# Kernel optimization log

Measured on AMD Instinct MI355X. Metric: run time of the kernel, lower is better.

## Reference

```python
import jax, jax.numpy as jnp
import numpy as np

B, IN, OUT, P = 512, 4096, 4096, 4
BITS = 4
MAX_INT = float(2 ** (BITS - 1) - 1)  # 7.0


def setup_inputs() -> dict:
    key = jax.random.key(0)
    k1, k2, k3, k4 = jax.random.split(key, 4)
    x = jax.random.normal(k1, (B, IN), dtype=jnp.float32)
    # Cached LFSR-generated pseudo-random matrix, values normalized to [-1, 1]
    U = jax.random.uniform(k2, (OUT * IN, P), dtype=jnp.float32, minval=-1.0, maxval=1.0)
    # 4-bit quantized projection: integers in [-7, 7] stored as float
    q = jnp.round(jnp.clip(jax.random.normal(k3, (P,), dtype=jnp.float32) * 3.0, -MAX_INT, MAX_INT))
    b = jax.random.normal(k4, (OUT,), dtype=jnp.float32)
    return {"x": x, "U": U, "q": q, "b": b, "exponent": 0}


def reference(x, U, q, b, exponent):
    # dequantize: t_hat = q / max_int * 2^exponent  (shared-exponent 4-bit dequant)
    scale = jnp.float32(2.0) ** exponent
    t_hat = q / MAX_INT * scale                      # [P]
    # reconstruct full weight: W = U @ t_hat, reshape to (out, in)
    w = (U @ t_hat).reshape(OUT, IN)                 # [OUT, IN]
    # original layer forward (nn.Linear): y = x @ W^T + b
    return x @ w.T + b                               # [B, OUT]
```

## Files before the change

kernel.cpp:

```cpp
#include <hip/hip_runtime.h>
#include <hip/hip_bf16.h>

typedef unsigned short ushort_t;
typedef unsigned int uint_t;
typedef __attribute__((ext_vector_type(4))) float f32x4;
typedef __attribute__((ext_vector_type(8))) short bf16x8;

#define B_DIM 512
#define IN_DIM 4096
#define OUT_DIM 4096
#define BN 64
#define BK 32
#define KSPLIT 8

__device__ __forceinline__ ushort_t f2bf(float f) {
    union { float f; uint_t u; } v; v.f = f;
    uint_t r = v.u + 0x7fffu + ((v.u >> 16) & 1u);
    return (ushort_t)(r >> 16);
}

__device__ __forceinline__ void async_copy16(void* lds, const void* g) {
    __builtin_amdgcn_global_load_lds(
        (const __attribute__((address_space(1))) uint_t*)g,
        (__attribute__((address_space(3))) uint_t*)lds, 16, 0, 0);
}

__global__ __launch_bounds__(256) void conv_x(const float4* __restrict__ X4,
                                              ushort_t* __restrict__ Xb) {
    size_t i = (size_t)blockIdx.x * 256 + threadIdx.x;
    float4 a = X4[i];
    ushort_t r[4] = { f2bf(a.x), f2bf(a.y), f2bf(a.z), f2bf(a.w) };
    *(uint2*)(Xb + i * 4) = *(const uint2*)r;
}

__global__ __launch_bounds__(256, 2) void gemm_fused(
    const ushort_t* __restrict__ Xb,
    const float4* __restrict__ U4,
    const float* __restrict__ q,
    const int* __restrict__ expo,
    float* __restrict__ part)
{
    const int K = IN_DIM, N = OUT_DIM, M = B_DIM;
    __shared__ ushort_t sX[512 * 32];
    __shared__ ushort_t sU[64 * 32];

    const int tid  = threadIdx.x;
    const int lane = tid & 63;
    const int wave = tid >> 6;
    const int n0 = blockIdx.x * BN;
    const int kz = blockIdx.y;
    const int kseg = K / KSPLIT;
    const size_t kbase = (size_t)kz * kseg;

    const float scale = exp2f((float)expo[0]) * (1.0f / 7.0f);
    const float t0 = q[0] * scale, t1 = q[1] * scale,
                t2 = q[2] * scale, t3 = q[3] * scale;

    const int xrow = tid >> 2;
    const int xcol = (tid & 3) * 8;
    const ushort_t* gx = Xb + (size_t)xrow * K + kbase + xcol;
    ushort_t* lx = sX + tid * 8;

    const int nb = tid >> 4;
    const int kp = tid & 15;
    const float4* gu = U4 + (size_t)(n0 + nb) * K + kbase + 2 * kp;
    uint_t* lu = (uint_t*)sU + nb * 16 + kp;

    const int quad = lane >> 4;
    const int r16  = lane & 15;
    const ushort_t* fa = sX + (wave * 128 + r16) * 32 + quad * 8;
    const ushort_t* fb = sU + r16 * 32 + quad * 8;

    f32x4 acc[8][4] = {};

    const int nsteps = kseg / BK;
    for (int s = 0; s < nsteps; ++s) {
#pragma unroll
        for (int p = 0; p < 8; ++p)
            async_copy16(lx + p * 2048, gx + (size_t)p * 64 * K);
        gx += BK;
#pragma unroll
        for (int r = 0; r < 4; ++r) {
            const float4* g = gu + (size_t)r * 16 * K;
            float4 ua = g[0], ub = g[1];
            float w0 = ua.x * t0 + ua.y * t1 + ua.z * t2 + ua.w * t3;
            float w1 = ub.x * t0 + ub.y * t1 + ub.z * t2 + ub.w * t3;
            lu[r * 256] = (uint_t)f2bf(w0) | ((uint_t)f2bf(w1) << 16);
        }
        gu += BK;
        __syncthreads();

        bf16x8 bv[4];
#pragma unroll
        for (int j = 0; j < 4; ++j)
            bv[j] = *(const bf16x8*)(fb + j * 16 * 32);
#pragma unroll
        for (int i = 0; i < 8; ++i) {
            bf16x8 av = *(const bf16x8*)(fa + i * 16 * 32);
#pragma unroll
            for (int j = 0; j < 4; ++j)
                acc[i][j] = __builtin_amdgcn_mfma_f32_16x16x32_bf16(
                    av, bv[j], acc[i][j], 0, 0, 0);
        }
        __syncthreads();
    }

    float* outp = part + (size_t)kz * M * N;
#pragma unroll
    for (int i = 0; i < 8; ++i) {
        const int mrow = wave * 128 + i * 16 + quad * 4;
#pragma unroll
        for (int j = 0; j < 4; ++j) {
            const int ncol = n0 + j * 16 + r16;
            float* o = outp + (size_t)mrow * N + ncol;
#pragma unroll
            for (int r = 0; r < 4; ++r)
                o[(size_t)r * N] = acc[i][j][r];
        }
    }
}

__global__ __launch_bounds__(256) void reduce_bias(const float4* __restrict__ part,
                                                   const float4* __restrict__ bias,
                                                   float4* __restrict__ out) {
    const int MN4 = (B_DIM * OUT_DIM) / 4;
    int i = blockIdx.x * 256 + threadIdx.x;
    float4 bb = bias[i & 1023];
    float sx = bb.x, sy = bb.y, sz = bb.z, sw = bb.w;
#pragma unroll
    for (int k = 0; k < KSPLIT; ++k) {
        float4 p = part[i + (size_t)k * MN4];
        sx += p.x; sy += p.y; sz += p.z; sw += p.w;
    }
    float4 o; o.x = sx; o.y = sy; o.z = sz; o.w = sw;
    out[i] = o;
}

extern "C" void kernel_launch(void* const* d_in, const int* in_sizes, int n_in,
                              void* d_out, int out_size, void* d_ws, size_t ws_size,
                              hipStream_t stream) {
    const float* x    = (const float*)d_in[0];
    const float* U    = (const float*)d_in[1];
    const float* q    = (const float*)d_in[2];
    const float* b    = (const float*)d_in[3];
    const int*   expo = (const int*)d_in[4];
    float* out = (float*)d_out;

    char* ws = (char*)d_ws;
    float*    prt = (float*)ws;
    ushort_t* Xb  = (ushort_t*)(ws + 67108864);

    conv_x<<<2048, 256, 0, stream>>>((const float4*)x, Xb);
    gemm_fused<<<dim3(64, KSPLIT), 256, 0, stream>>>(Xb, (const float4*)U,
                                                     q, expo, prt);
    reduce_bias<<<2048, 256, 0, stream>>>((const float4*)prt, (const float4*)b,
                                          (float4*)out);
}
```

Baseline: 418.8 us.

## Widen GEMM tile to 128 columns with 512 threads and store bf16 partials

The fused GEMM block grows from 64 to 128 output columns and from 256 to 512 threads arranged as a 4x2 wave grid, so each X tile loaded into LDS feeds twice as many columns. This halves the number of blocks and the total X traffic. The split-K partial sums are now written as bf16 instead of fp32, halving partial write and reduce-read traffic. In exchange, partials are rounded to bf16 before the reduction, which adds accuracy loss, and the grid drops to 256 blocks, which may reduce occupancy on a 256-CU device.

```diff
diff --git a/kernel.cpp b/kernel.cpp
--- a/kernel.cpp
+++ b/kernel.cpp
@@ -9,7 +9,7 @@
 #define B_DIM 512
 #define IN_DIM 4096
 #define OUT_DIM 4096
-#define BN 64
+#define BN 128
 #define BK 32
 #define KSPLIT 8
 
@@ -33,20 +33,22 @@
     *(uint2*)(Xb + i * 4) = *(const uint2*)r;
 }
 
-__global__ __launch_bounds__(256, 2) void gemm_fused(
+__global__ __launch_bounds__(512, 2) void gemm_fused(
     const ushort_t* __restrict__ Xb,
     const float4* __restrict__ U4,
     const float* __restrict__ q,
     const int* __restrict__ expo,
-    float* __restrict__ part)
+    ushort_t* __restrict__ part)
 {
     const int K = IN_DIM, N = OUT_DIM, M = B_DIM;
     __shared__ ushort_t sX[512 * 32];
-    __shared__ ushort_t sU[64 * 32];
+    __shared__ ushort_t sU[128 * 32];
 
     const int tid  = threadIdx.x;
     const int lane = tid & 63;
     const int wave = tid >> 6;
+    const int wrow = (wave & 3) * 128;
+    const int wcol = (wave >> 2) * 64;
     const int n0 = blockIdx.x * BN;
     const int kz = blockIdx.y;
     const int kseg = K / KSPLIT;
@@ -68,24 +70,24 @@
 
     const int quad = lane >> 4;
     const int r16  = lane & 15;
-    const ushort_t* fa = sX + (wave * 128 + r16) * 32 + quad * 8;
-    const ushort_t* fb = sU + r16 * 32 + quad * 8;
+    const ushort_t* fa = sX + (wrow + r16) * 32 + quad * 8;
+    const ushort_t* fb = sU + (wcol + r16) * 32 + quad * 8;
 
     f32x4 acc[8][4] = {};
 
     const int nsteps = kseg / BK;
     for (int s = 0; s < nsteps; ++s) {
 #pragma unroll
-        for (int p = 0; p < 8; ++p)
-            async_copy16(lx + p * 2048, gx + (size_t)p * 64 * K);
+        for (int p = 0; p < 4; ++p)
+            async_copy16(lx + p * 4096, gx + (size_t)p * 128 * K);
         gx += BK;
 #pragma unroll
         for (int r = 0; r < 4; ++r) {
-            const float4* g = gu + (size_t)r * 16 * K;
+            const float4* g = gu + (size_t)r * 32 * K;
             float4 ua = g[0], ub = g[1];
             float w0 = ua.x * t0 + ua.y * t1 + ua.z * t2 + ua.w * t3;
             float w1 = ub.x * t0 + ub.y * t1 + ub.z * t2 + ub.w * t3;
-            lu[r * 256] = (uint_t)f2bf(w0) | ((uint_t)f2bf(w1) << 16);
+            lu[r * 512] = (uint_t)f2bf(w0) | ((uint_t)f2bf(w1) << 16);
         }
         gu += BK;
         __syncthreads();
@@ -105,22 +107,22 @@
         __syncthreads();
     }
 
-    float* outp = part + (size_t)kz * M * N;
+    ushort_t* outp = part + (size_t)kz * M * N;
 #pragma unroll
     for (int i = 0; i < 8; ++i) {
-        const int mrow = wave * 128 + i * 16 + quad * 4;
+        const int mrow = wrow + i * 16 + quad * 4;
 #pragma unroll
         for (int j = 0; j < 4; ++j) {
-            const int ncol = n0 + j * 16 + r16;
-            float* o = outp + (size_t)mrow * N + ncol;
+            const int ncol = n0 + wcol + j * 16 + r16;
+            ushort_t* o = outp + (size_t)mrow * N + ncol;
 #pragma unroll
             for (int r = 0; r < 4; ++r)
-                o[(size_t)r * N] = acc[i][j][r];
+                o[(size_t)r * N] = f2bf(acc[i][j][r]);
         }
     }
 }
 
-__global__ __launch_bounds__(256) void reduce_bias(const float4* __restrict__ part,
+__global__ __launch_bounds__(256) void reduce_bias(const uint2* __restrict__ partb,
                                                    const float4* __restrict__ bias,
                                                    float4* __restrict__ out) {
     const int MN4 = (B_DIM * OUT_DIM) / 4;
@@ -129,8 +131,11 @@
     float sx = bb.x, sy = bb.y, sz = bb.z, sw = bb.w;
 #pragma unroll
     for (int k = 0; k < KSPLIT; ++k) {
-        float4 p = part[i + (size_t)k * MN4];
-        sx += p.x; sy += p.y; sz += p.z; sw += p.w;
+        uint2 p = partb[i + (size_t)k * MN4];
+        sx += __uint_as_float(p.x << 16);
+        sy += __uint_as_float(p.x & 0xffff0000u);
+        sz += __uint_as_float(p.y << 16);
+        sw += __uint_as_float(p.y & 0xffff0000u);
     }
     float4 o; o.x = sx; o.y = sy; o.z = sz; o.w = sw;
     out[i] = o;
@@ -147,12 +152,12 @@
     float* out = (float*)d_out;
 
     char* ws = (char*)d_ws;
-    float*    prt = (float*)ws;
-    ushort_t* Xb  = (ushort_t*)(ws + 67108864);
+    ushort_t* prtb = (ushort_t*)ws;
+    ushort_t* Xb   = (ushort_t*)(ws + 33554432);
 
     conv_x<<<2048, 256, 0, stream>>>((const float4*)x, Xb);
-    gemm_fused<<<dim3(64, KSPLIT), 256, 0, stream>>>(Xb, (const float4*)U,
-                                                     q, expo, prt);
-    reduce_bias<<<2048, 256, 0, stream>>>((const float4*)prt, (const float4*)b,
+    gemm_fused<<<dim3(32, KSPLIT), 512, 0, stream>>>(Xb, (const float4*)U,
+                                                     q, expo, prtb);
+    reduce_bias<<<2048, 256, 0, stream>>>((const uint2*)prtb, (const float4*)b,
                                           (float4*)out);
 }
```

New measurement: 415.6 us. No clear change (-0.8%).
